# Performance work log

Measured on AMD Instinct MI355X. Metric: run time of the kernel, lower is better.

## Reference

```python
import jax, jax.numpy as jnp
import numpy as np

DIM = 1024
HEADS = 16
DIM_HEAD = 64
INNER = HEADS * DIM_HEAD
SCALE = DIM_HEAD ** -0.5


def rotate_half(t):
    # '... (j d) -> ... j d' with j=2: split last dim in half
    x1, x2 = jnp.split(t, 2, axis=-1)
    return jnp.concatenate((-x2, x1), axis=-1)


def rotary_pos(n, d, dtype):
    inv_freq = 1.0 / (10000.0 ** (jnp.arange(0, d, 2, dtype=jnp.float32) / d))
    freqs = jnp.arange(n, dtype=jnp.float32)[:, None] * inv_freq[None, :]  # (n, d/2)
    return jnp.concatenate((freqs, freqs), axis=-1).astype(dtype)  # (n, d)


def apply_rope(pos, t):
    return t * jnp.cos(pos) + rotate_half(t) * jnp.sin(pos)


def setup_inputs() -> dict:
    key = jax.random.key(0)
    ks = jax.random.split(key, 5)
    x = jax.random.normal(ks[0], (2, 2048, DIM), dtype=jnp.float32)
    gamma = jnp.ones((DIM,), dtype=jnp.float32)
    beta = jnp.zeros((DIM,), dtype=jnp.float32)
    Wq = jax.random.normal(ks[1], (DIM, INNER), dtype=jnp.float32) * 0.02
    Wkv = jax.random.normal(ks[2], (DIM, 2 * INNER), dtype=jnp.float32) * 0.02
    Wo = jax.random.normal(ks[3], (INNER, DIM), dtype=jnp.float32) * 0.02
    return {"x": x, "gamma": gamma, "beta": beta, "Wq": Wq, "Wkv": Wkv, "Wo": Wo}


def reference(x, gamma, beta, Wq, Wkv, Wo):
    b, n, _ = x.shape
    # LayerNorm with learned gamma, fixed-zero beta buffer
    mu = jnp.mean(x, axis=-1, keepdims=True)
    var = jnp.var(x, axis=-1, keepdims=True)
    xn = (x - mu) / jnp.sqrt(var + 1e-5) * gamma + beta

    q = xn @ Wq                       # (b, n, inner)
    kv = xn @ Wkv
    k, v = jnp.split(kv, 2, axis=-1)

    def to_heads(t):
        return t.reshape(b, n, HEADS, DIM_HEAD).transpose(0, 2, 1, 3)  # b h n d

    q, k, v = map(to_heads, (q, k, v))

    pos = rotary_pos(n, DIM_HEAD, x.dtype)  # (n, d)
    q = apply_rope(pos, q)
    k = apply_rope(pos, k)

    q = q * SCALE
    sim = jnp.einsum('bhid,bhjd->bhij', q, k)

    neg = -jnp.finfo(sim.dtype).max
    causal_mask = jnp.triu(jnp.ones((n, n), dtype=bool), k=1)
    sim = jnp.where(causal_mask, neg, sim)

    attn = jax.nn.softmax(sim, axis=-1)
    out = jnp.einsum('bhij,bhjd->bhid', attn, v)
    out = out.transpose(0, 2, 1, 3).reshape(b, n, INNER)
    return out @ Wo
```

## Files before the change

kernel.cpp:

```cpp
#include <hip/hip_runtime.h>
#include <stdint.h>

typedef unsigned short u16;
typedef __attribute__((ext_vector_type(8))) short short8;
typedef __attribute__((ext_vector_type(4))) float floatx4;
typedef __attribute__((ext_vector_type(4))) unsigned short u16x4;
typedef __attribute__((ext_vector_type(2))) unsigned int uint2v;

__device__ __forceinline__ float bf2f(u16 v) {
  union { uint32_t u; float f; } x; x.u = ((uint32_t)v) << 16; return x.f;
}
__device__ __forceinline__ u16 f2bf(float f) {
  union { float f; uint32_t u; } x; x.f = f;
  uint32_t r = x.u + 0x7fffu + ((x.u >> 16) & 1u);
  return (u16)(r >> 16);
}
__device__ __forceinline__ uint32_t fu(float f) {
  union { float f; uint32_t u; } x; x.f = f; return x.u;
}

#define GL2LDS(g, l)                                                          \
  __builtin_amdgcn_global_load_lds(                                           \
      (const __attribute__((address_space(1))) void*)(g),                     \
      (__attribute__((address_space(3))) void*)(l), 16, 0, 0)

#define WAITBAR(N)                                                            \
  asm volatile("s_waitcnt vmcnt(" #N ")\n\ts_barrier" ::: "memory")
#define BARX asm volatile("s_barrier" ::: "memory")
#define VM0BARX asm volatile("s_waitcnt vmcnt(0)\n\ts_barrier" ::: "memory")

__global__ __launch_bounds__(256) void prep_k(const float* __restrict__ x,
                                              const float* __restrict__ gamma,
                                              const float* __restrict__ beta,
                                              const float* __restrict__ Wq,
                                              const float* __restrict__ Wkv,
                                              const float* __restrict__ Wo,
                                              u16* __restrict__ xn,
                                              u16* __restrict__ wqkvT,
                                              u16* __restrict__ woT) {
  int bid = blockIdx.x;
  int t = threadIdx.x;
  if (bid < 4096) {
    int row = bid;
    const float* xr = x + (size_t)row * 1024;
    float4 xv = *(const float4*)(xr + t * 4);
    float v0 = xv.x, v1 = xv.y, v2 = xv.z, v3 = xv.w;
    float s = v0 + v1 + v2 + v3;
    float s2 = v0 * v0 + v1 * v1 + v2 * v2 + v3 * v3;
#pragma unroll
    for (int d = 1; d < 64; d <<= 1) {
      s += __shfl_xor(s, d, 64);
      s2 += __shfl_xor(s2, d, 64);
    }
    __shared__ float red[8];
    int lane = t & 63, wv = t >> 6;
    if (lane == 0) { red[wv] = s; red[4 + wv] = s2; }
    __syncthreads();
    s = red[0] + red[1] + red[2] + red[3];
    s2 = red[4] + red[5] + red[6] + red[7];
    float mu = s * (1.0f / 1024.0f);
    float var = s2 * (1.0f / 1024.0f) - mu * mu;
    float rstd = rsqrtf(var + 1e-5f);
    float4 gv = *(const float4*)(gamma + t * 4);
    float4 bv = *(const float4*)(beta + t * 4);
    u16x4 ov;
    ov.x = f2bf((v0 - mu) * rstd * gv.x + bv.x);
    ov.y = f2bf((v1 - mu) * rstd * gv.y + bv.y);
    ov.z = f2bf((v2 - mu) * rstd * gv.z + bv.z);
    ov.w = f2bf((v3 - mu) * rstd * gv.w + bv.w);
    *(u16x4*)(xn + (size_t)row * 1024 + t * 4) = ov;
  } else {
    __shared__ float tile[32][33];
    int wb = bid - 4096;
    const float* in;
    u16* outp;
    int C;
    if (wb < 1024) { in = Wq; outp = wqkvT; C = 1024; }
    else if (wb < 3072) { wb -= 1024; in = Wkv; outp = wqkvT + 1024 * 1024; C = 2048; }
    else { wb -= 3072; in = Wo; outp = woT; C = 1024; }
    int nbx = C >> 5;
    int c0 = (wb % nbx) * 32, r0 = (wb / nbx) * 32;
    int tx = t & 31, ty = t >> 5;
#pragma unroll
    for (int i = 0; i < 32; i += 8)
      tile[ty + i][tx] = in[(size_t)(r0 + ty + i) * C + c0 + tx];
    __syncthreads();
#pragma unroll
    for (int i = 0; i < 32; i += 8)
      outp[(size_t)(c0 + ty + i) * 1024 + r0 + tx] = f2bf(tile[tx][ty + i]);
  }
}

__global__ __launch_bounds__(512, 2) void gemm_qkv_k(const u16* __restrict__ A,
                                                     const u16* __restrict__ BT,
                                                     u16* __restrict__ C) {
  __shared__ __align__(16) u16 sA[2][16384];
  __shared__ __align__(16) u16 sB[2][16384];
  int tid = threadIdx.x;
  int w = tid >> 6, l = tid & 63;
  int lr = l & 15, lq = l >> 4;
  int wr = w >> 2, wc = w & 3;
  int bm = blockIdx.y * 256;
  int bn = blockIdx.x * 256;
  floatx4 acc[8][4] = {};
  int rl = w * 8 + (l >> 3);
  int scol = ((l & 7) ^ ((l >> 3) & 7)) * 8;
  int w512l8 = w * 512 + l * 8;
  const u16* gA = A + (size_t)(bm + rl) * 1024 + scol;
  const u16* gB = BT + (size_t)(bn + rl) * 1024 + scol;
  int aab = wr * 8192 + lr * 64;
  int bbb = (wc >> 1) * 8192 + ((wc & 1) * 64 + lr) * 64;
  int cs0 = (lq * 8) ^ ((lr & 7) << 3);
  int cs1 = (32 + lq * 8) ^ ((lr & 7) << 3);

#define ST_A(bi)                                                              \
  { GL2LDS(gA, &sA[bi][w512l8]);                                              \
    GL2LDS(gA + 65536, &sA[bi][4096 + w512l8]);                               \
    GL2LDS(gA + 131072, &sA[bi][8192 + w512l8]);                              \
    GL2LDS(gA + 196608, &sA[bi][12288 + w512l8]); }
#define ST_B0(bi)                                                             \
  { GL2LDS(gB, &sB[bi][w512l8]);                                              \
    GL2LDS(gB + 65536, &sB[bi][4096 + w512l8]); }
#define ST_B1(bi)                                                             \
  { GL2LDS(gB + 131072, &sB[bi][8192 + w512l8]);                              \
    GL2LDS(gB + 196608, &sB[bi][12288 + w512l8]); }
#define LDA4(bi, qm, cc)                                                      \
  { af[0] = *(const short8*)&sA[bi][aab + (qm)*4096 + 0 + (cc)];              \
    af[1] = *(const short8*)&sA[bi][aab + (qm)*4096 + 1024 + (cc)];           \
    af[2] = *(const short8*)&sA[bi][aab + (qm)*4096 + 2048 + (cc)];           \
    af[3] = *(const short8*)&sA[bi][aab + (qm)*4096 + 3072 + (cc)]; }
#define LDB4(bi, cc)                                                          \
  { bf[0] = *(const short8*)&sB[bi][bbb + 0 + (cc)];                          \
    bf[1] = *(const short8*)&sB[bi][bbb + 1024 + (cc)];                       \
    bf[2] = *(const short8*)&sB[bi][bbb + 2048 + (cc)];                       \
    bf[3] = *(const short8*)&sB[bi][bbb + 3072 + (cc)]; }
#define MM16(qm)                                                              \
  _Pragma("unroll") for (int mi = 0; mi < 4; mi++)                            \
  _Pragma("unroll") for (int ni = 0; ni < 4; ni++)                            \
      acc[(qm)*4 + mi][ni] = __builtin_amdgcn_mfma_f32_16x16x32_bf16(         \
          af[mi], bf[ni], acc[(qm)*4 + mi][ni], 0, 0, 0);
#define KT(p, q, DOST)                                                        \
  {                                                                           \
    short8 af[4], bf[4];                                                      \
    LDA4(p, 0, cs0); LDB4(p, cs0);                                            \
    if (DOST) ST_A(q);                                                        \
    BARX; __builtin_amdgcn_s_setprio(1); MM16(0);                             \
    __builtin_amdgcn_s_setprio(0); BARX;                                      \
    LDA4(p, 1, cs0);                                                          \
    if (DOST) ST_B0(q);                                                       \
    BARX; __builtin_amdgcn_s_setprio(1); MM16(1);                             \
    __builtin_amdgcn_s_setprio(0); BARX;                                      \
    LDA4(p, 0, cs1); LDB4(p, cs1);                                            \
    if (DOST) ST_B1(q);                                                       \
    BARX; __builtin_amdgcn_s_setprio(1); MM16(0);                             \
    __builtin_amdgcn_s_setprio(0); BARX;                                      \
    LDA4(p, 1, cs1);                                                          \
    if (DOST) { gA += 64; gB += 64; }                                         \
    BARX; __builtin_amdgcn_s_setprio(1); MM16(1);                             \
    __builtin_amdgcn_s_setprio(0); VM0BARX;                                   \
  }

  ST_A(0); ST_B0(0); ST_B1(0);
  gA += 64; gB += 64;
  VM0BARX;
#pragma unroll 1
  for (int t = 0; t < 7; ++t) {
    KT(0, 1, 1);
    KT(1, 0, 1);
  }
  KT(0, 1, 1);
  KT(1, 0, 0);

  int sec = bn >> 10;
  if (sec == 2) {
#pragma unroll
    for (int am = 0; am < 8; am++)
#pragma unroll
      for (int ni = 0; ni < 4; ni++) {
        int col = bn + wc * 64 + ni * 16 + lr;
        int cv = col - 2048;
        int row = bm + wr * 128 + (am >> 2) * 64 + (am & 3) * 16 + lq * 4;
        int bq = row >> 11;
        int n = row & 2047;
        int bh = (bq << 4) | (cv >> 6);
        int d = cv & 63;
        size_t L = ((size_t)(bh * 64 + d) << 11) + n;
        u16x4 ov;
        ov.x = f2bf(acc[am][ni][0]);
        ov.y = f2bf(acc[am][ni][1]);
        ov.z = f2bf(acc[am][ni][2]);
        ov.w = f2bf(acc[am][ni][3]);
        *(u16x4*)(C + (L >> 10) * 3072 + 2048 + (L & 1023)) = ov;
      }
  } else {
    float QS = (sec == 0) ? 0.125f * 1.44269504088896f : 1.0f;
#pragma unroll
    for (int ni = 0; ni < 2; ni++) {
      int i = ni * 16 + lr;
      float invf = exp2f(-(float)i * 0.4152410118609203f);
#pragma unroll
      for (int am = 0; am < 8; am++)
#pragma unroll
        for (int r = 0; r < 4; r++) {
          int row = bm + wr * 128 + (am >> 2) * 64 + (am & 3) * 16 + lq * 4 + r;
          int n = row & 2047;
          float ang = (float)n * invf;
          float s_, c_;
          __sincosf(ang, &s_, &c_);
          float x1 = acc[am][ni][r], x2 = acc[am][ni + 2][r];
          int col = bn + wc * 64 + ni * 16 + lr;
          C[(size_t)row * 3072 + col] = f2bf((x1 * c_ - x2 * s_) * QS);
          C[(size_t)row * 3072 + col + 32] = f2bf((x2 * c_ + x1 * s_) * QS);
        }
    }
  }
}

__global__ __launch_bounds__(256) void gemm64_bf16_k(const u16* __restrict__ A,
                                                     const u16* __restrict__ BT,
                                                     float* __restrict__ C,
                                                     int K, int lda, int ldc) {
  __shared__ __align__(16) u16 lA[3][64 * 32];
  __shared__ __align__(16) u16 lB[3][128 * 32];
  int tid = threadIdx.x;
  int bm = blockIdx.y * 64;
  int bn = blockIdx.x * 128;
  int w = tid >> 6, l = tid & 63;
  int wm = (w >> 1) * 32, wn = (w & 1) * 64;
  int lr = l & 15, lq = l >> 4;
  floatx4 acc[2][4] = {};
  int sr = w * 16 + (l >> 2);
  int sc = (l & 3) * 8;
  int sds = sr * 32 + sc;
  const u16* pA0 = A + (size_t)(bm + sr) * lda + sc;
  const u16* pB0 = BT + (size_t)(bn + sr) * K + sc;
  const u16* pB1 = pB0 + (size_t)64 * K;
  int ao[2], bo[4];
#pragma unroll
  for (int i = 0; i < 2; i++) ao[i] = (wm + i * 16 + lr) * 32 + lq * 8;
#pragma unroll
  for (int i = 0; i < 4; i++) bo[i] = (wn + i * 16 + lr) * 32 + lq * 8;

#define STAGE_O(bi)                                                           \
  {                                                                           \
    GL2LDS(pA0, &lA[bi][sds]);                                                \
    GL2LDS(pB0, &lB[bi][sds]);                                                \
    GL2LDS(pB1, &lB[bi][sds + 2048]);                                         \
    pA0 += 32; pB0 += 32; pB1 += 32;                                          \
  }
#define COMPUTE_O(bi)                                                         \
  {                                                                           \
    short8 afr[2], bfr[4];                                                    \
    _Pragma("unroll") for (int i = 0; i < 2; i++)                             \
        afr[i] = *(const short8*)(&lA[bi][ao[i]]);                            \
    _Pragma("unroll") for (int i = 0; i < 4; i++)                             \
        bfr[i] = *(const short8*)(&lB[bi][bo[i]]);                            \
    _Pragma("unroll") for (int mi = 0; mi < 2; mi++)                          \
        _Pragma("unroll") for (int ni = 0; ni < 4; ni++)                      \
            acc[mi][ni] = __builtin_amdgcn_mfma_f32_16x16x32_bf16(            \
                afr[mi], bfr[ni], acc[mi][ni], 0, 0, 0);                      \
  }

  STAGE_O(0);
  STAGE_O(1);
#pragma unroll 1
  for (int t = 0; t < 10; ++t) {
    WAITBAR(3); STAGE_O(2); COMPUTE_O(0);
    WAITBAR(3); STAGE_O(0); COMPUTE_O(1);
    WAITBAR(3); STAGE_O(1); COMPUTE_O(2);
  }
  WAITBAR(3); COMPUTE_O(0);
  WAITBAR(0); COMPUTE_O(1);

#pragma unroll
  for (int mi = 0; mi < 2; mi++)
#pragma unroll
    for (int ni = 0; ni < 4; ni++)
#pragma unroll
      for (int r = 0; r < 4; r++) {
        int row = bm + wm + mi * 16 + lq * 4 + r;
        int col = bn + wn + ni * 16 + lr;
        C[(size_t)row * ldc + col] = acc[mi][ni][r];
      }
}

#define LPT 64
#define FIXM 4.0f
__device__ __forceinline__ void attn_tile2(const u16* lK, const u16* lV, u16* lp,
                                           const short8* aq, floatx4* o,
                                           float& l_i, int lr, int lq,
                                           bool diag, int q0, int k0g,
                                           short8 ones) {
  floatx4 s[4];
#pragma unroll
  for (int ni = 0; ni < 4; ni++) {
    floatx4 a = {};
#pragma unroll
    for (int kc = 0; kc < 2; kc++) {
      int R = ni * 16 + lr;
      int c8 = (kc * 4 + lq) ^ (R & 7);
      short8 kf = *(const short8*)&lK[R * 64 + c8 * 8];
      a = __builtin_amdgcn_mfma_f32_16x16x32_bf16(kf, aq[kc], a, 0, 0, 0);
    }
    s[ni] = a;
  }
  if (diag) {
    int qg = q0 + lr;
#pragma unroll
    for (int ni = 0; ni < 4; ni++)
#pragma unroll
      for (int r = 0; r < 4; r++) {
        int kg = k0g + ni * 16 + lq * 4 + r;
        if (kg > qg) s[ni][r] = -1e30f;
      }
  }
  int swz = (lr & 7) << 3;
#pragma unroll
  for (int ni = 0; ni < 4; ni++) {
    float p0 = exp2f(s[ni][0] - FIXM), p1 = exp2f(s[ni][1] - FIXM);
    float p2 = exp2f(s[ni][2] - FIXM), p3 = exp2f(s[ni][3] - FIXM);
    uint2v dw;
    dw.x = __builtin_amdgcn_perm(fu(p1), fu(p0), 0x07060302u);
    dw.y = __builtin_amdgcn_perm(fu(p3), fu(p2), 0x07060302u);
    *(uint2v*)&lp[lr * LPT + ((ni * 16 + lq * 4) ^ swz)] = dw;
  }
  short8 pb0 = *(const short8*)&lp[lr * LPT + ((lq * 8) ^ swz)];
  short8 pb1 = *(const short8*)&lp[lr * LPT + ((32 + lq * 8) ^ swz)];
  floatx4 z = {};
  z = __builtin_amdgcn_mfma_f32_16x16x32_bf16(ones, pb0, z, 0, 0, 0);
  z = __builtin_amdgcn_mfma_f32_16x16x32_bf16(ones, pb1, z, 0, 0, 0);
  l_i += z[0];
#pragma unroll
  for (int di = 0; di < 4; di++) {
    int R = di * 16 + lr;
    int c80 = lq ^ (R & 7);
    int c81 = (4 + lq) ^ (R & 7);
    short8 v0 = *(const short8*)&lV[R * 64 + c80 * 8];
    o[di] = __builtin_amdgcn_mfma_f32_16x16x32_bf16(v0, pb0, o[di], 0, 0, 0);
    short8 v1 = *(const short8*)&lV[R * 64 + c81 * 8];
    o[di] = __builtin_amdgcn_mfma_f32_16x16x32_bf16(v1, pb1, o[di], 0, 0, 0);
  }
}

__global__ __launch_bounds__(256) void attn_k(const u16* __restrict__ qkv,
                                              u16* __restrict__ out) {
  __shared__ __align__(16) u16 lK[2][64 * 64];
  __shared__ __align__(16) u16 lV[2][64 * 64];
  __shared__ __align__(16) u16 lP[4][16 * LPT];
  int bh = blockIdx.x;
  int b = bh >> 4, h = bh & 15;
  int y = blockIdx.y;
  int g = y >> 3, o_ = y & 7;
  int j = (g & 1) ? ((g << 3) + 7 - o_) : y;
  int tid = threadIdx.x;
  int w = tid >> 6, l = tid & 63;
  int lr = l & 15, lq = l >> 4;
  int q0 = j * 64 + w * 16;
  const u16* qb = qkv + (size_t)b * 2048 * 3072 + h * 64;
  const u16* kb = qkv + (size_t)b * 2048 * 3072 + 1024 + h * 64;
  int bh64 = bh * 64;
  short8 aq[2];
  aq[0] = *(const short8*)(qb + (size_t)(q0 + lr) * 3072 + lq * 8);
  aq[1] = *(const short8*)(qb + (size_t)(q0 + lr) * 3072 + 32 + lq * 8);
  short8 ones;
#pragma unroll
  for (int i = 0; i < 8; i++) ones[i] = (short)0x3F80;
  floatx4 o[4] = {};
  float l_ = 0.0f;
  int srow8 = l >> 3;
  int sc8 = (l & 7) ^ srow8;
  u16* lp = &lP[w][0];
  auto stage = [&](int bufi, int kt) {
#pragma unroll
    for (int c = 0; c < 2; c++) {
      int m = w + c * 4;
      int row = m * 8 + srow8;
      GL2LDS(kb + (size_t)(kt * 64 + row) * 3072 + sc8 * 8, &lK[bufi][m * 512]);
      int nn = kt * 64 + sc8 * 8;
      GL2LDS(qkv + (size_t)((bh64 + row) * 2 + (nn >> 10)) * 3072 + 2048 +
                 (nn & 1023),
             &lV[bufi][m * 512]);
    }
  };
  stage(0, 0);
  for (int kt = 0; kt <= j; ++kt) {
    int cur = kt & 1;
    __syncthreads();
    if (kt < j) stage(cur ^ 1, kt + 1);
    attn_tile2(lK[cur], lV[cur], lp, aq, o, l_, lr, lq, kt == j, q0, kt * 64,
               ones);
  }
  float rl = 1.0f / l_;
#pragma unroll
  for (int di = 0; di < 4; di++) {
    uint2v dw;
    u16 a0 = f2bf(o[di][0] * rl), a1 = f2bf(o[di][1] * rl);
    u16 a2 = f2bf(o[di][2] * rl), a3 = f2bf(o[di][3] * rl);
    dw.x = (uint32_t)a0 | ((uint32_t)a1 << 16);
    dw.y = (uint32_t)a2 | ((uint32_t)a3 << 16);
    int dcol = h * 64 + di * 16 + lq * 4;
    *(uint2v*)(out + ((size_t)(b * 2048 + q0 + lr)) * 1024 + dcol) = dw;
  }
}

extern "C" void kernel_launch(void* const* d_in, const int* in_sizes, int n_in,
                              void* d_out, int out_size, void* d_ws, size_t ws_size,
                              hipStream_t stream) {
  const float* x = (const float*)d_in[0];
  const float* gamma = (const float*)d_in[1];
  const float* beta = (const float*)d_in[2];
  const float* Wq = (const float*)d_in[3];
  const float* Wkv = (const float*)d_in[4];
  const float* Wo = (const float*)d_in[5];
  float* out = (float*)d_out;
  char* ws = (char*)d_ws;

  u16* qkv = (u16*)(ws);
  u16* wqkvT = (u16*)(ws + 25165824);
  u16* woT = (u16*)(ws + 31457280);
  u16* xn = (u16*)(ws + 33554432);
  u16* attn_out = xn;

  prep_k<<<8192, 256, 0, stream>>>(x, gamma, beta, Wq, Wkv, Wo, xn, wqkvT, woT);
  gemm_qkv_k<<<dim3(12, 16), 512, 0, stream>>>(xn, wqkvT, qkv);
  attn_k<<<dim3(32, 32), 256, 0, stream>>>(qkv, attn_out);
  gemm64_bf16_k<<<dim3(8, 64), 256, 0, stream>>>(attn_out, woT, out, 1024, 1024, 1024);
}
```

Measured before the change: 192.2 us.

## Process two 16-row query tiles per wave in attention, halving block size

Each wave in the attention kernel now computes 32 query rows as two 16-row tiles sharing each K and V fragment loaded from LDS, and the block shrinks to two waves. Staging work per thread doubles to cover the same 64-key tile. This reduces LDS read traffic per MFMA but lowers waves per block and raises register pressure. The constant exponent offset before exp2 is also removed, which cancels in normalisation but slightly increases overflow risk for large scores.

```diff
diff --git a/kernel.cpp b/kernel.cpp
--- a/kernel.cpp
+++ b/kernel.cpp
@@ -285,68 +285,87 @@
 }
 
 #define LPT 64
-#define FIXM 4.0f
-__device__ __forceinline__ void attn_tile2(const u16* lK, const u16* lV, u16* lp,
-                                           const short8* aq, floatx4* o,
-                                           float& l_i, int lr, int lq,
-                                           bool diag, int q0, int k0g,
-                                           short8 ones) {
-  floatx4 s[4];
+__device__ __forceinline__ void attn_step2(const u16* lK, const u16* lV, u16* lp,
+                                           const short8* aqA, const short8* aqB,
+                                           floatx4* oA, floatx4* oB,
+                                           float& lA_, float& lB_,
+                                           int lr, int lq, bool diag, int q0,
+                                           int k0g, short8 ones) {
+  floatx4 sA[4], sB[4];
 #pragma unroll
   for (int ni = 0; ni < 4; ni++) {
-    floatx4 a = {};
+    floatx4 a = {}, b = {};
 #pragma unroll
     for (int kc = 0; kc < 2; kc++) {
       int R = ni * 16 + lr;
       int c8 = (kc * 4 + lq) ^ (R & 7);
       short8 kf = *(const short8*)&lK[R * 64 + c8 * 8];
-      a = __builtin_amdgcn_mfma_f32_16x16x32_bf16(kf, aq[kc], a, 0, 0, 0);
+      a = __builtin_amdgcn_mfma_f32_16x16x32_bf16(kf, aqA[kc], a, 0, 0, 0);
+      b = __builtin_amdgcn_mfma_f32_16x16x32_bf16(kf, aqB[kc], b, 0, 0, 0);
     }
-    s[ni] = a;
+    sA[ni] = a;
+    sB[ni] = b;
   }
   if (diag) {
-    int qg = q0 + lr;
+    int qgA = q0 + lr, qgB = q0 + 16 + lr;
 #pragma unroll
     for (int ni = 0; ni < 4; ni++)
 #pragma unroll
       for (int r = 0; r < 4; r++) {
         int kg = k0g + ni * 16 + lq * 4 + r;
-        if (kg > qg) s[ni][r] = -1e30f;
+        if (kg > qgA) sA[ni][r] = -1e30f;
+        if (kg > qgB) sB[ni][r] = -1e30f;
       }
   }
   int swz = (lr & 7) << 3;
 #pragma unroll
   for (int ni = 0; ni < 4; ni++) {
-    float p0 = exp2f(s[ni][0] - FIXM), p1 = exp2f(s[ni][1] - FIXM);
-    float p2 = exp2f(s[ni][2] - FIXM), p3 = exp2f(s[ni][3] - FIXM);
-    uint2v dw;
-    dw.x = __builtin_amdgcn_perm(fu(p1), fu(p0), 0x07060302u);
-    dw.y = __builtin_amdgcn_perm(fu(p3), fu(p2), 0x07060302u);
-    *(uint2v*)&lp[lr * LPT + ((ni * 16 + lq * 4) ^ swz)] = dw;
-  }
-  short8 pb0 = *(const short8*)&lp[lr * LPT + ((lq * 8) ^ swz)];
-  short8 pb1 = *(const short8*)&lp[lr * LPT + ((32 + lq * 8) ^ swz)];
+    uint2v dwA, dwB;
+    dwA.x = __builtin_amdgcn_perm(fu(exp2f(sA[ni][1])), fu(exp2f(sA[ni][0])),
+                                  0x07060302u);
+    dwA.y = __builtin_amdgcn_perm(fu(exp2f(sA[ni][3])), fu(exp2f(sA[ni][2])),
+                                  0x07060302u);
+    dwB.x = __builtin_amdgcn_perm(fu(exp2f(sB[ni][1])), fu(exp2f(sB[ni][0])),
+                                  0x07060302u);
+    dwB.y = __builtin_amdgcn_perm(fu(exp2f(sB[ni][3])), fu(exp2f(sB[ni][2])),
+                                  0x07060302u);
+    int off = lr * LPT + ((ni * 16 + lq * 4) ^ swz);
+    *(uint2v*)&lp[off] = dwA;
+    *(uint2v*)&lp[1024 + off] = dwB;
+  }
+  int ro0 = lr * LPT + ((lq * 8) ^ swz);
+  int ro1 = lr * LPT + ((32 + lq * 8) ^ swz);
+  short8 pa0 = *(const short8*)&lp[ro0];
+  short8 pa1 = *(const short8*)&lp[ro1];
+  short8 pb0 = *(const short8*)&lp[1024 + ro0];
+  short8 pb1 = *(const short8*)&lp[1024 + ro1];
   floatx4 z = {};
-  z = __builtin_amdgcn_mfma_f32_16x16x32_bf16(ones, pb0, z, 0, 0, 0);
-  z = __builtin_amdgcn_mfma_f32_16x16x32_bf16(ones, pb1, z, 0, 0, 0);
-  l_i += z[0];
+  z = __builtin_amdgcn_mfma_f32_16x16x32_bf16(ones, pa0, z, 0, 0, 0);
+  z = __builtin_amdgcn_mfma_f32_16x16x32_bf16(ones, pa1, z, 0, 0, 0);
+  lA_ += z[0];
+  floatx4 z2 = {};
+  z2 = __builtin_amdgcn_mfma_f32_16x16x32_bf16(ones, pb0, z2, 0, 0, 0);
+  z2 = __builtin_amdgcn_mfma_f32_16x16x32_bf16(ones, pb1, z2, 0, 0, 0);
+  lB_ += z2[0];
 #pragma unroll
   for (int di = 0; di < 4; di++) {
     int R = di * 16 + lr;
     int c80 = lq ^ (R & 7);
     int c81 = (4 + lq) ^ (R & 7);
     short8 v0 = *(const short8*)&lV[R * 64 + c80 * 8];
-    o[di] = __builtin_amdgcn_mfma_f32_16x16x32_bf16(v0, pb0, o[di], 0, 0, 0);
+    oA[di] = __builtin_amdgcn_mfma_f32_16x16x32_bf16(v0, pa0, oA[di], 0, 0, 0);
+    oB[di] = __builtin_amdgcn_mfma_f32_16x16x32_bf16(v0, pb0, oB[di], 0, 0, 0);
     short8 v1 = *(const short8*)&lV[R * 64 + c81 * 8];
-    o[di] = __builtin_amdgcn_mfma_f32_16x16x32_bf16(v1, pb1, o[di], 0, 0, 0);
-  }
-}
-
-__global__ __launch_bounds__(256) void attn_k(const u16* __restrict__ qkv,
+    oA[di] = __builtin_amdgcn_mfma_f32_16x16x32_bf16(v1, pa1, oA[di], 0, 0, 0);
+    oB[di] = __builtin_amdgcn_mfma_f32_16x16x32_bf16(v1, pb1, oB[di], 0, 0, 0);
+  }
+}
+
+__global__ __launch_bounds__(128) void attn_k(const u16* __restrict__ qkv,
                                               u16* __restrict__ out) {
   __shared__ __align__(16) u16 lK[2][64 * 64];
   __shared__ __align__(16) u16 lV[2][64 * 64];
-  __shared__ __align__(16) u16 lP[4][16 * LPT];
+  __shared__ __align__(16) u16 lP[4096];
   int bh = blockIdx.x;
   int b = bh >> 4, h = bh & 15;
   int y = blockIdx.y;
@@ -355,25 +374,29 @@
   int tid = threadIdx.x;
   int w = tid >> 6, l = tid & 63;
   int lr = l & 15, lq = l >> 4;
-  int q0 = j * 64 + w * 16;
+  int q0 = j * 64 + w * 32;
   const u16* qb = qkv + (size_t)b * 2048 * 3072 + h * 64;
   const u16* kb = qkv + (size_t)b * 2048 * 3072 + 1024 + h * 64;
   int bh64 = bh * 64;
-  short8 aq[2];
-  aq[0] = *(const short8*)(qb + (size_t)(q0 + lr) * 3072 + lq * 8);
-  aq[1] = *(const short8*)(qb + (size_t)(q0 + lr) * 3072 + 32 + lq * 8);
+  short8 aqA[2], aqB[2];
+#pragma unroll
+  for (int kc = 0; kc < 2; kc++) {
+    aqA[kc] = *(const short8*)(qb + (size_t)(q0 + lr) * 3072 + kc * 32 + lq * 8);
+    aqB[kc] =
+        *(const short8*)(qb + (size_t)(q0 + 16 + lr) * 3072 + kc * 32 + lq * 8);
+  }
   short8 ones;
 #pragma unroll
   for (int i = 0; i < 8; i++) ones[i] = (short)0x3F80;
-  floatx4 o[4] = {};
-  float l_ = 0.0f;
+  floatx4 oA[4] = {}, oB[4] = {};
+  float lA_ = 0.0f, lB_ = 0.0f;
   int srow8 = l >> 3;
   int sc8 = (l & 7) ^ srow8;
-  u16* lp = &lP[w][0];
+  u16* lp = &lP[w * 2048];
   auto stage = [&](int bufi, int kt) {
 #pragma unroll
-    for (int c = 0; c < 2; c++) {
-      int m = w + c * 4;
+    for (int c = 0; c < 4; c++) {
+      int m = w * 4 + c;
       int row = m * 8 + srow8;
       GL2LDS(kb + (size_t)(kt * 64 + row) * 3072 + sc8 * 8, &lK[bufi][m * 512]);
       int nn = kt * 64 + sc8 * 8;
@@ -387,19 +410,24 @@
     int cur = kt & 1;
     __syncthreads();
     if (kt < j) stage(cur ^ 1, kt + 1);
-    attn_tile2(lK[cur], lV[cur], lp, aq, o, l_, lr, lq, kt == j, q0, kt * 64,
-               ones);
-  }
-  float rl = 1.0f / l_;
+    attn_step2(lK[cur], lV[cur], lp, aqA, aqB, oA, oB, lA_, lB_, lr, lq,
+               kt == j, q0, kt * 64, ones);
+  }
+  float rlA = 1.0f / lA_, rlB = 1.0f / lB_;
 #pragma unroll
   for (int di = 0; di < 4; di++) {
-    uint2v dw;
-    u16 a0 = f2bf(o[di][0] * rl), a1 = f2bf(o[di][1] * rl);
-    u16 a2 = f2bf(o[di][2] * rl), a3 = f2bf(o[di][3] * rl);
-    dw.x = (uint32_t)a0 | ((uint32_t)a1 << 16);
-    dw.y = (uint32_t)a2 | ((uint32_t)a3 << 16);
+    uint2v dwA, dwB;
+    u16 a0 = f2bf(oA[di][0] * rlA), a1 = f2bf(oA[di][1] * rlA);
+    u16 a2 = f2bf(oA[di][2] * rlA), a3 = f2bf(oA[di][3] * rlA);
+    dwA.x = (uint32_t)a0 | ((uint32_t)a1 << 16);
+    dwA.y = (uint32_t)a2 | ((uint32_t)a3 << 16);
+    u16 b0 = f2bf(oB[di][0] * rlB), b1 = f2bf(oB[di][1] * rlB);
+    u16 b2 = f2bf(oB[di][2] * rlB), b3 = f2bf(oB[di][3] * rlB);
+    dwB.x = (uint32_t)b0 | ((uint32_t)b1 << 16);
+    dwB.y = (uint32_t)b2 | ((uint32_t)b3 << 16);
     int dcol = h * 64 + di * 16 + lq * 4;
-    *(uint2v*)(out + ((size_t)(b * 2048 + q0 + lr)) * 1024 + dcol) = dw;
+    *(uint2v*)(out + ((size_t)(b * 2048 + q0 + lr)) * 1024 + dcol) = dwA;
+    *(uint2v*)(out + ((size_t)(b * 2048 + q0 + 16 + lr)) * 1024 + dcol) = dwB;
   }
 }
 
@@ -423,6 +451,6 @@
 
   prep_k<<<8192, 256, 0, stream>>>(x, gamma, beta, Wq, Wkv, Wo, xn, wqkvT, woT);
   gemm_qkv_k<<<dim3(12, 16), 512, 0, stream>>>(xn, wqkvT, qkv);
-  attn_k<<<dim3(32, 32), 256, 0, stream>>>(qkv, attn_out);
+  attn_k<<<dim3(32, 32), 128, 0, stream>>>(qkv, attn_out);
   gemm64_bf16_k<<<dim3(8, 64), 256, 0, stream>>>(attn_out, woT, out, 1024, 1024, 1024);
 }
```

Result: slower. 207.7 us (+8.1%).

## Switch QKV GEMM to triple-buffered 32-wide K tiles with partial vmcnt waits

Applied to the files above, without the earlier changes.

The QKV projection GEMM now stages K in 32-element slices across three LDS buffers instead of 64-element slices across two. Each tile waits with vmcnt(4) rather than draining all outstanding loads, so one prefetch stays in flight while the next tile computes. The LDS swizzle and addressing are reworked for 32-wide rows. This trades more barriers and loop iterations per unit of K for less LDS use and deeper overlap of global loads with MFMA work.

```diff
diff --git a/kernel.cpp b/kernel.cpp
--- a/kernel.cpp
+++ b/kernel.cpp
@@ -27,7 +27,6 @@
 #define WAITBAR(N)                                                            \
   asm volatile("s_waitcnt vmcnt(" #N ")\n\ts_barrier" ::: "memory")
 #define BARX asm volatile("s_barrier" ::: "memory")
-#define VM0BARX asm volatile("s_waitcnt vmcnt(0)\n\ts_barrier" ::: "memory")
 
 __global__ __launch_bounds__(256) void prep_k(const float* __restrict__ x,
                                               const float* __restrict__ gamma,
@@ -94,8 +93,8 @@
 __global__ __launch_bounds__(512, 2) void gemm_qkv_k(const u16* __restrict__ A,
                                                      const u16* __restrict__ BT,
                                                      u16* __restrict__ C) {
-  __shared__ __align__(16) u16 sA[2][16384];
-  __shared__ __align__(16) u16 sB[2][16384];
+  __shared__ __align__(16) u16 sA[3][8192];
+  __shared__ __align__(16) u16 sB[3][8192];
   int tid = threadIdx.x;
   int w = tid >> 6, l = tid & 63;
   int lr = l & 15, lq = l >> 4;
@@ -103,73 +102,58 @@
   int bm = blockIdx.y * 256;
   int bn = blockIdx.x * 256;
   floatx4 acc[8][4] = {};
-  int rl = w * 8 + (l >> 3);
-  int scol = ((l & 7) ^ ((l >> 3) & 7)) * 8;
-  int w512l8 = w * 512 + l * 8;
-  const u16* gA = A + (size_t)(bm + rl) * 1024 + scol;
-  const u16* gB = BT + (size_t)(bn + rl) * 1024 + scol;
-  int aab = wr * 8192 + lr * 64;
-  int bbb = (wc >> 1) * 8192 + ((wc & 1) * 64 + lr) * 64;
-  int cs0 = (lq * 8) ^ ((lr & 7) << 3);
-  int cs1 = (32 + lq * 8) ^ ((lr & 7) << 3);
-
-#define ST_A(bi)                                                              \
-  { GL2LDS(gA, &sA[bi][w512l8]);                                              \
-    GL2LDS(gA + 65536, &sA[bi][4096 + w512l8]);                               \
-    GL2LDS(gA + 131072, &sA[bi][8192 + w512l8]);                              \
-    GL2LDS(gA + 196608, &sA[bi][12288 + w512l8]); }
-#define ST_B0(bi)                                                             \
-  { GL2LDS(gB, &sB[bi][w512l8]);                                              \
-    GL2LDS(gB + 65536, &sB[bi][4096 + w512l8]); }
-#define ST_B1(bi)                                                             \
-  { GL2LDS(gB + 131072, &sB[bi][8192 + w512l8]);                              \
-    GL2LDS(gB + 196608, &sB[bi][12288 + w512l8]); }
-#define LDA4(bi, qm, cc)                                                      \
-  { af[0] = *(const short8*)&sA[bi][aab + (qm)*4096 + 0 + (cc)];              \
-    af[1] = *(const short8*)&sA[bi][aab + (qm)*4096 + 1024 + (cc)];           \
-    af[2] = *(const short8*)&sA[bi][aab + (qm)*4096 + 2048 + (cc)];           \
-    af[3] = *(const short8*)&sA[bi][aab + (qm)*4096 + 3072 + (cc)]; }
-#define LDB4(bi, cc)                                                          \
-  { bf[0] = *(const short8*)&sB[bi][bbb + 0 + (cc)];                          \
-    bf[1] = *(const short8*)&sB[bi][bbb + 1024 + (cc)];                       \
-    bf[2] = *(const short8*)&sB[bi][bbb + 2048 + (cc)];                       \
-    bf[3] = *(const short8*)&sB[bi][bbb + 3072 + (cc)]; }
+  int srow = tid >> 2;
+  int scol = ((tid & 3) ^ (srow & 3)) * 8;
+  int t8 = tid * 8;
+  const u16* gA = A + (size_t)(bm + srow) * 1024 + scol;
+  const u16* gB = BT + (size_t)(bn + srow) * 1024 + scol;
+  int csr = (lq ^ (lr & 3)) * 8;
+  int aab = (wr * 128 + lr) * 32 + csr;
+  int bbb = (wc * 64 + lr) * 32 + csr;
+
+#define ST_A32(bi)                                                            \
+  { GL2LDS(gA, &sA[bi][t8]); GL2LDS(gA + 131072, &sA[bi][4096 + t8]); }
+#define ST_B32(bi)                                                            \
+  { GL2LDS(gB, &sB[bi][t8]); GL2LDS(gB + 131072, &sB[bi][4096 + t8]); }
+#define LDA32(bi, qm)                                                         \
+  { af[0] = *(const short8*)&sA[bi][aab + (qm)*2048 + 0];                     \
+    af[1] = *(const short8*)&sA[bi][aab + (qm)*2048 + 512];                   \
+    af[2] = *(const short8*)&sA[bi][aab + (qm)*2048 + 1024];                  \
+    af[3] = *(const short8*)&sA[bi][aab + (qm)*2048 + 1536]; }
+#define LDB32(bi)                                                             \
+  { bf[0] = *(const short8*)&sB[bi][bbb + 0];                                 \
+    bf[1] = *(const short8*)&sB[bi][bbb + 512];                               \
+    bf[2] = *(const short8*)&sB[bi][bbb + 1024];                              \
+    bf[3] = *(const short8*)&sB[bi][bbb + 1536]; }
 #define MM16(qm)                                                              \
   _Pragma("unroll") for (int mi = 0; mi < 4; mi++)                            \
   _Pragma("unroll") for (int ni = 0; ni < 4; ni++)                            \
       acc[(qm)*4 + mi][ni] = __builtin_amdgcn_mfma_f32_16x16x32_bf16(         \
           af[mi], bf[ni], acc[(qm)*4 + mi][ni], 0, 0, 0);
-#define KT(p, q, DOST)                                                        \
+#define KT32(p, q, DOST, ENDW)                                                \
   {                                                                           \
     short8 af[4], bf[4];                                                      \
-    LDA4(p, 0, cs0); LDB4(p, cs0);                                            \
-    if (DOST) ST_A(q);                                                        \
+    LDA32(p, 0); LDB32(p);                                                    \
+    if (DOST) ST_A32(q);                                                      \
     BARX; __builtin_amdgcn_s_setprio(1); MM16(0);                             \
     __builtin_amdgcn_s_setprio(0); BARX;                                      \
-    LDA4(p, 1, cs0);                                                          \
-    if (DOST) ST_B0(q);                                                       \
+    LDA32(p, 1);                                                              \
+    if (DOST) { ST_B32(q); gA += 32; gB += 32; }                              \
     BARX; __builtin_amdgcn_s_setprio(1); MM16(1);                             \
-    __builtin_amdgcn_s_setprio(0); BARX;                                      \
-    LDA4(p, 0, cs1); LDB4(p, cs1);                                            \
-    if (DOST) ST_B1(q);                                                       \
-    BARX; __builtin_amdgcn_s_setprio(1); MM16(0);                             \
-    __builtin_amdgcn_s_setprio(0); BARX;                                      \
-    LDA4(p, 1, cs1);                                                          \
-    if (DOST) { gA += 64; gB += 64; }                                         \
-    BARX; __builtin_amdgcn_s_setprio(1); MM16(1);                             \
-    __builtin_amdgcn_s_setprio(0); VM0BARX;                                   \
-  }
-
-  ST_A(0); ST_B0(0); ST_B1(0);
-  gA += 64; gB += 64;
-  VM0BARX;
+    __builtin_amdgcn_s_setprio(0); ENDW;                                      \
+  }
+
+  ST_A32(0); ST_B32(0); gA += 32; gB += 32;
+  ST_A32(1); ST_B32(1); gA += 32; gB += 32;
+  WAITBAR(4);
 #pragma unroll 1
-  for (int t = 0; t < 7; ++t) {
-    KT(0, 1, 1);
-    KT(1, 0, 1);
-  }
-  KT(0, 1, 1);
-  KT(1, 0, 0);
+  for (int t = 0; t < 10; ++t) {
+    KT32(0, 2, 1, WAITBAR(4));
+    KT32(1, 0, 1, WAITBAR(4));
+    KT32(2, 1, 1, WAITBAR(4));
+  }
+  KT32(0, 2, 0, WAITBAR(0));
+  KT32(1, 2, 0, BARX);
 
   int sec = bn >> 10;
   if (sec == 2) {
```

Result: no change. 191.6 us (-0.4%).
